# Kernel optimization log

Measured on AMD Instinct MI355X. Metric: run time of the kernel, lower is better.

Reference implementation:

```python
import jax, jax.numpy as jnp
import numpy as np

N = 100000
E = 1600000
F_FEAT, F_COND, F_HID, F_LAT = 128, 32, 128, 64


def setup_inputs() -> dict:
    key = jax.random.key(0)
    ks = jax.random.split(key, 16)
    feature = jax.random.normal(ks[0], (N, F_FEAT), dtype=jnp.float32)
    condition = jax.random.normal(ks[1], (N, F_COND), dtype=jnp.float32)
    edge_index = jax.random.randint(ks[2], (2, E), 0, N, dtype=jnp.int64)

    def glorot(k, fan_in, fan_out):
        s = jnp.sqrt(6.0 / (fan_in + fan_out)).astype(jnp.float32)
        return jax.random.uniform(k, (fan_in, fan_out), jnp.float32, -s, s)

    enc_in = F_FEAT + F_COND   # 160
    dec_in = F_LAT + F_COND    # 96
    return {
        "feature": feature,
        "condition": condition,
        "edge_index": edge_index,
        "W_e1": glorot(ks[3], enc_in, F_HID), "b_e1": jnp.zeros((F_HID,), jnp.float32),
        "W_e2": glorot(ks[4], F_HID, F_HID), "b_e2": jnp.zeros((F_HID,), jnp.float32),
        "W_e3": glorot(ks[5], F_HID, F_LAT), "b_e3": jnp.zeros((F_LAT,), jnp.float32),
        "W_d1": glorot(ks[6], dec_in, F_HID), "b_d1": jnp.zeros((F_HID,), jnp.float32),
        "W_d2": glorot(ks[7], F_HID, F_HID), "b_d2": jnp.zeros((F_HID,), jnp.float32),
        "W_d3": glorot(ks[8], F_HID, F_FEAT), "b_d3": jnp.zeros((F_FEAT,), jnp.float32),
    }


def _gcn_conv(x, W, b, src, dst, dinv):
    # GCNConv with add_self_loops=True, symmetric normalization:
    # out = D^{-1/2} (A + I) D^{-1/2} X W + b
    h = x @ W                                        # [N, out]
    coef = (dinv[src] * dinv[dst])[:, None]          # [E, 1]
    msg = h[src] * coef                              # [E, out]
    agg = jax.ops.segment_sum(msg, dst, num_segments=x.shape[0])
    agg = agg + h * (dinv * dinv)[:, None]           # self-loop term
    return agg + b


def reference(feature, condition, edge_index,
              W_e1, b_e1, W_e2, b_e2, W_e3, b_e3,
              W_d1, b_d1, W_d2, b_d2, W_d3, b_d3):
    src, dst = edge_index[0], edge_index[1]
    n = feature.shape[0]
    # degree with self loops (edge weights = 1)
    deg = jax.ops.segment_sum(jnp.ones((src.shape[0],), jnp.float32), dst,
                              num_segments=n) + 1.0
    dinv = jax.lax.rsqrt(deg)

    # encoder
    x = jnp.concatenate([feature, condition], axis=1)
    h = jnp.tanh(_gcn_conv(x, W_e1, b_e1, src, dst, dinv))
    h = jnp.tanh(_gcn_conv(h, W_e2, b_e2, src, dst, dinv))
    z = _gcn_conv(h, W_e3, b_e3, src, dst, dinv)

    # decoder
    x = jnp.concatenate([z, condition], axis=1)
    h = jnp.tanh(_gcn_conv(x, W_d1, b_d1, src, dst, dinv))
    h = jnp.tanh(_gcn_conv(h, W_d2, b_d2, src, dst, dinv))
    out = _gcn_conv(h, W_d3, b_d3, src, dst, dinv)
    return out
```

## Files before the change

kernel.cpp:

```cpp
#include <hip/hip_runtime.h>
#include <hip/hip_fp16.h>
#include <math.h>

#define NN 100000
#define NE 1600000
#define NB ((NN + 255) >> 8)
#define CHUNK 8192
#define CAP 8192

typedef __attribute__((ext_vector_type(4))) float floatx4;
typedef __attribute__((ext_vector_type(8))) short shortx8;


__global__ __launch_bounds__(256)
void coarse_hist(const int* __restrict__ ei, int* __restrict__ bucket_cnt, int E) {
    __shared__ int h[512];
    int t = threadIdx.x;
    for (int i = t; i < 512; i += 256) h[i] = 0;
    __syncthreads();
    int base = blockIdx.x * CHUNK;
    int lim = min(base + CHUNK, E);
    for (int e = base + t; e < lim; e += 256) {
        int d = ei[E + e];
        atomicAdd(&h[d >> 8], 1);
    }
    __syncthreads();
    for (int i = t; i < 512; i += 256)
        if (h[i]) atomicAdd(&bucket_cnt[i], h[i]);
}

__global__ void scan_buckets(const int* __restrict__ bucket_cnt,
                             int* __restrict__ bucket_base,
                             int* __restrict__ bucket_fill) {
    __shared__ int sh[512];
    int t = threadIdx.x;
    int v = (t < NB) ? bucket_cnt[t] : 0;
    sh[t] = v;
    __syncthreads();
    for (int off = 1; off < 512; off <<= 1) {
        int u = (t >= off) ? sh[t - off] : 0;
        __syncthreads();
        sh[t] += u;
        __syncthreads();
    }
    int ex = (t == 0) ? 0 : sh[t - 1];
    if (t <= NB) bucket_base[t] = ex;
    if (t < NB) bucket_fill[t] = ex;
}

__global__ __launch_bounds__(256)
void coarse_scatter(const int* __restrict__ ei, int* __restrict__ bucket_fill,
                    unsigned long long* __restrict__ pairs, int E) {
    __shared__ int h[512];
    __shared__ int base[512];
    int t = threadIdx.x;
    for (int i = t; i < 512; i += 256) h[i] = 0;
    __syncthreads();
    int cbase = blockIdx.x * CHUNK;
    int lim = min(cbase + CHUNK, E);
    for (int e = cbase + t; e < lim; e += 256) {
        int d = ei[E + e];
        atomicAdd(&h[d >> 8], 1);
    }
    __syncthreads();
    for (int i = t; i < 512; i += 256)
        base[i] = h[i] ? atomicAdd(&bucket_fill[i], h[i]) : 0;
    __syncthreads();
    for (int i = t; i < 512; i += 256) h[i] = 0;
    __syncthreads();
    for (int e = cbase + t; e < lim; e += 256) {
        int s = ei[e];
        int d = ei[E + e];
        int b = d >> 8;
        int r = atomicAdd(&h[b], 1);
        pairs[base[b] + r] =
            ((unsigned long long)(unsigned)d << 32) | (unsigned)s;
    }
}

__global__ __launch_bounds__(256)
void fine_csr(const unsigned long long* __restrict__ pairs,
              const int* __restrict__ bucket_base,
              int* __restrict__ rowptr, int* __restrict__ colid,
              float* __restrict__ dinv, int n) {
    __shared__ int hist[256];
    __shared__ int offs[256];
    __shared__ int rank[256];
    __shared__ int lbuf[CAP];
    int b = blockIdx.x, t = threadIdx.x;
    int beg = bucket_base[b], end = bucket_base[b + 1];
    int cnt = end - beg;
    hist[t] = 0; rank[t] = 0;
    __syncthreads();
    for (int i = t; i < cnt; i += 256) {
        int d = (int)(pairs[beg + i] >> 32);
        atomicAdd(&hist[d & 255], 1);
    }
    __syncthreads();
    int v = hist[t];
    offs[t] = v;
    __syncthreads();
    for (int off = 1; off < 256; off <<= 1) {
        int u = (t >= off) ? offs[t - off] : 0;
        __syncthreads();
        offs[t] += u;
        __syncthreads();
    }
    int ex = (t == 0) ? 0 : offs[t - 1];
    int node = (b << 8) + t;
    if (node < n) {
        rowptr[node] = beg + ex;
        dinv[node] = rsqrtf((float)v + 1.0f);
    } else if (node == n) {
        rowptr[n] = beg + ex;
    }
    __syncthreads();
    offs[t] = ex;
    __syncthreads();
    for (int i = t; i < cnt; i += 256) {
        unsigned long long p = pairs[beg + i];
        int d = (int)(p >> 32) & 255;
        int s = (int)(p & 0xffffffffu);
        int r = atomicAdd(&rank[d], 1);
        lbuf[offs[d] + r] = s;
    }
    __syncthreads();
    for (int i = t; i < cnt; i += 256) colid[beg + i] = lbuf[i];
}


__device__ __forceinline__ void wsplit_one(const float* __restrict__ W,
                                           unsigned short* __restrict__ Wsw,
                                           int i, int K, int OUT) {
    int k = i / OUT, o = i % OUT;
    float w = W[i];
    unsigned u = __float_as_uint(w);
    float r = w - __uint_as_float(u & 0xFFFF0000u);
    int NT = OUT >> 4;
    int ktc = k >> 5, q = (k >> 3) & 3, j = k & 7;
    int nt = o >> 4, mm = o & 15;
    int lane = (q << 4) | mm;
    size_t base = ((((size_t)(ktc * NT + nt) * 2) * 64 + lane) << 3) + j;
    Wsw[base] = (unsigned short)(u >> 16);
    Wsw[base + 512] = (unsigned short)(__float_as_uint(r) >> 16);
}

__global__ __launch_bounds__(256)
void wsplit_all(const float* __restrict__ W0, unsigned short* __restrict__ O0,
                const float* __restrict__ W1, unsigned short* __restrict__ O1,
                const float* __restrict__ W2, unsigned short* __restrict__ O2,
                const float* __restrict__ W3, unsigned short* __restrict__ O3,
                const float* __restrict__ W4, unsigned short* __restrict__ O4,
                const float* __restrict__ W5, unsigned short* __restrict__ O5) {
    int i = blockIdx.x * 256 + threadIdx.x;
    if (i < 20480) { wsplit_one(W0, O0, i, 160, 128); return; }
    i -= 20480;
    if (i < 16384) { wsplit_one(W1, O1, i, 128, 128); return; }
    i -= 16384;
    if (i < 8192)  { wsplit_one(W2, O2, i, 128, 64);  return; }
    i -= 8192;
    if (i < 12288) { wsplit_one(W3, O3, i, 96, 128);  return; }
    i -= 12288;
    if (i < 16384) { wsplit_one(W4, O4, i, 128, 128); return; }
    i -= 16384;
    if (i < 16384) { wsplit_one(W5, O5, i, 128, 128); }
}


__device__ __forceinline__ void split8(const float* v, shortx8& hi, shortx8& lo) {
#pragma unroll
    for (int i = 0; i < 8; i++) {
        unsigned u = __float_as_uint(v[i]);
        float r = v[i] - __uint_as_float(u & 0xFFFF0000u);
        hi[i] = (short)(u >> 16);
        lo[i] = (short)(__float_as_uint(r) >> 16);
    }
}

template <int OUT, int K, int K1>
__global__ __launch_bounds__(512, 4)
void gemm_mfma(const float* __restrict__ X1, const float* __restrict__ X2,
               const unsigned short* __restrict__ Wsw,
               const float* __restrict__ dinv,
               __half* __restrict__ Y, int ntiles) {
    constexpr int NT = OUT / 16;
    constexpr int NKTC = K / 32;
    constexpr int K2 = K - K1;
    constexpr int PERC = OUT * 128;
    constexpr int CSZ = (65536 / PERC < NKTC) ? (65536 / PERC) : NKTC;
    __shared__ __align__(16) unsigned short lds[CSZ * PERC / 2];

    const int t = threadIdx.x;
    const int wave = t >> 6, lane = t & 63;
    const int m = lane & 15, q = lane >> 4;
    const int tile0 = blockIdx.x * 16 + wave * 2;
    const int tile1 = tile0 + 1;
    const bool act0 = tile0 < ntiles;
    const bool act1 = tile1 < ntiles;
    const int r0 = act0 ? tile0 * 16 + m : 0;
    const int r1 = act1 ? tile1 * 16 + m : 0;
    const float* ap1a = X1 + (size_t)r0 * K1 + q * 8;
    const float* ap1b = X1 + (size_t)r1 * K1 + q * 8;
    const float* ap2a = (K2 > 0) ? (X2 + (size_t)r0 * K2 + q * 8) : X1;
    const float* ap2b = (K2 > 0) ? (X2 + (size_t)r1 * K2 + q * 8) : X1;

    floatx4 acc0[NT], acc1[NT];
#pragma unroll
    for (int nt = 0; nt < NT; nt++) {
        acc0[nt] = (floatx4){0.f, 0.f, 0.f, 0.f};
        acc1[nt] = (floatx4){0.f, 0.f, 0.f, 0.f};
    }

#pragma unroll
    for (int c0 = 0; c0 < NKTC; c0 += CSZ) {
        const int cl = (NKTC - c0 < CSZ) ? (NKTC - c0) : CSZ;
        if (c0 != 0) __syncthreads();
        {
            const float4* gs = (const float4*)Wsw + (size_t)c0 * (PERC / 16);
            float4* ld = (float4*)lds;
            int tot = cl * (PERC / 16);
            for (int i = t; i < tot; i += 512) ld[i] = gs[i];
        }
        __syncthreads();
#pragma unroll
        for (int ktc = 0; ktc < cl; ktc++) {
            const int kg = (c0 + ktc) * 32;
            const float* pa = (kg < K1) ? (ap1a + kg) : (ap2a + (kg - K1));
            const float* pb = (kg < K1) ? (ap1b + kg) : (ap2b + (kg - K1));
            float av0[8], av1[8];
            *(float4*)&av0[0] = *(const float4*)(pa);
            *(float4*)&av0[4] = *(const float4*)(pa + 4);
            *(float4*)&av1[0] = *(const float4*)(pb);
            *(float4*)&av1[4] = *(const float4*)(pb + 4);
            shortx8 ahi0, alo0, ahi1, alo1;
            split8(av0, ahi0, alo0);
            split8(av1, ahi1, alo1);
#pragma unroll
            for (int nt = 0; nt < NT; nt++) {
                const unsigned short* fb =
                    lds + ((((ktc * NT + nt) * 2) * 64 + lane) << 3);
                shortx8 bhi = *(const shortx8*)fb;
                shortx8 blo = *(const shortx8*)(fb + 512);
                acc0[nt] = __builtin_amdgcn_mfma_f32_16x16x32_bf16(ahi0, bhi, acc0[nt], 0, 0, 0);
                acc1[nt] = __builtin_amdgcn_mfma_f32_16x16x32_bf16(ahi1, bhi, acc1[nt], 0, 0, 0);
                acc0[nt] = __builtin_amdgcn_mfma_f32_16x16x32_bf16(ahi0, blo, acc0[nt], 0, 0, 0);
                acc1[nt] = __builtin_amdgcn_mfma_f32_16x16x32_bf16(ahi1, blo, acc1[nt], 0, 0, 0);
                acc0[nt] = __builtin_amdgcn_mfma_f32_16x16x32_bf16(alo0, bhi, acc0[nt], 0, 0, 0);
                acc1[nt] = __builtin_amdgcn_mfma_f32_16x16x32_bf16(alo1, bhi, acc1[nt], 0, 0, 0);
            }
        }
    }

    if (act0) {
        float di[4];
#pragma unroll
        for (int r = 0; r < 4; r++) di[r] = dinv[tile0 * 16 + q * 4 + r];
#pragma unroll
        for (int nt = 0; nt < NT; nt++) {
#pragma unroll
            for (int r = 0; r < 4; r++) {
                int orow = tile0 * 16 + q * 4 + r;
                Y[(size_t)orow * OUT + nt * 16 + m] =
                    __float2half_rn(acc0[nt][r] * di[r]);
            }
        }
    }
    if (act1) {
        float di[4];
#pragma unroll
        for (int r = 0; r < 4; r++) di[r] = dinv[tile1 * 16 + q * 4 + r];
#pragma unroll
        for (int nt = 0; nt < NT; nt++) {
#pragma unroll
            for (int r = 0; r < 4; r++) {
                int orow = tile1 * 16 + q * 4 + r;
                Y[(size_t)orow * OUT + nt * 16 + m] =
                    __float2half_rn(acc1[nt][r] * di[r]);
            }
        }
    }
}


template <int OUT, bool TANH>
__global__ __launch_bounds__(256)
void prop_row(const __half2* __restrict__ hs, const float* __restrict__ dinv,
              const int* __restrict__ rowptr, const int* __restrict__ colid,
              const float* __restrict__ bias, float* __restrict__ out,
              int ldo, int n) {
    constexpr int LPR = OUT / 4;
    constexpr int G = 64 / LPR;
    constexpr int RS2 = OUT / 4;

    int wave = threadIdx.x >> 6, lane = threadIdx.x & 63;
    int node = blockIdx.x * 4 + wave;
    if (node >= n) return;
    int g = lane / LPR, fq = lane % LPR;
    int beg = rowptr[node], end = rowptr[node + 1];
    const float2* __restrict__ b2 = (const float2*)hs;

    float ax = 0.f, ay = 0.f, az = 0.f, aw = 0.f;
    int e = beg;
    for (; e + 8 * G <= end; e += 8 * G) {
        int s[8];
#pragma unroll
        for (int j = 0; j < 8; j++) s[j] = colid[e + j * G + g];
        float2 v[8];
#pragma unroll
        for (int j = 0; j < 8; j++) v[j] = b2[(size_t)s[j] * RS2 + fq];
#pragma unroll
        for (int j = 0; j < 8; j++) {
            float2 f0 = __half22float2(*(const __half2*)&v[j].x);
            float2 f1 = __half22float2(*(const __half2*)&v[j].y);
            ax += f0.x; ay += f0.y; az += f1.x; aw += f1.y;
        }
    }
    if (e + 4 * G <= end) {
        int s[4];
#pragma unroll
        for (int j = 0; j < 4; j++) s[j] = colid[e + j * G + g];
        float2 v[4];
#pragma unroll
        for (int j = 0; j < 4; j++) v[j] = b2[(size_t)s[j] * RS2 + fq];
#pragma unroll
        for (int j = 0; j < 4; j++) {
            float2 f0 = __half22float2(*(const __half2*)&v[j].x);
            float2 f1 = __half22float2(*(const __half2*)&v[j].y);
            ax += f0.x; ay += f0.y; az += f1.x; aw += f1.y;
        }
        e += 4 * G;
    }
    for (; e + G <= end; e += G) {
        int s = colid[e + g];
        float2 v = b2[(size_t)s * RS2 + fq];
        float2 f0 = __half22float2(*(const __half2*)&v.x);
        float2 f1 = __half22float2(*(const __half2*)&v.y);
        ax += f0.x; ay += f0.y; az += f1.x; aw += f1.y;
    }
    if (e + g < end) {
        int s = colid[e + g];
        float2 v = b2[(size_t)s * RS2 + fq];
        float2 f0 = __half22float2(*(const __half2*)&v.x);
        float2 f1 = __half22float2(*(const __half2*)&v.y);
        ax += f0.x; ay += f0.y; az += f1.x; aw += f1.y;
    }

    if constexpr (G >= 2) {
        ax += __shfl_xor(ax, LPR); ay += __shfl_xor(ay, LPR);
        az += __shfl_xor(az, LPR); aw += __shfl_xor(aw, LPR);
    }
    if constexpr (G == 4) {
        ax += __shfl_xor(ax, 2 * LPR); ay += __shfl_xor(ay, 2 * LPR);
        az += __shfl_xor(az, 2 * LPR); aw += __shfl_xor(aw, 2 * LPR);
    }

    if (g == 0) {
        float2 sv = b2[(size_t)node * RS2 + fq];
        float2 f0 = __half22float2(*(const __half2*)&sv.x);
        float2 f1 = __half22float2(*(const __half2*)&sv.y);
        ax += f0.x; ay += f0.y; az += f1.x; aw += f1.y;
        float di = dinv[node];
        float4 bb = *(const float4*)(bias + fq * 4);
        float ox = di * ax + bb.x;
        float oy = di * ay + bb.y;
        float oz = di * az + bb.z;
        float ow = di * aw + bb.w;
        if (TANH) { ox = tanhf(ox); oy = tanhf(oy); oz = tanhf(oz); ow = tanhf(ow); }
        *(float4*)(out + (size_t)node * ldo + fq * 4) = make_float4(ox, oy, oz, ow);
    }
}


extern "C" void kernel_launch(void* const* d_in, const int* in_sizes, int n_in,
                              void* d_out, int out_size, void* d_ws, size_t ws_size,
                              hipStream_t stream) {
    const int n = NN, E = NE;
    const float* feature   = (const float*)d_in[0];
    const float* condition = (const float*)d_in[1];
    const int*   ei        = (const int*)d_in[2];
    const float* W_e1 = (const float*)d_in[3];  const float* b_e1 = (const float*)d_in[4];
    const float* W_e2 = (const float*)d_in[5];  const float* b_e2 = (const float*)d_in[6];
    const float* W_e3 = (const float*)d_in[7];  const float* b_e3 = (const float*)d_in[8];
    const float* W_d1 = (const float*)d_in[9];  const float* b_d1 = (const float*)d_in[10];
    const float* W_d2 = (const float*)d_in[11]; const float* b_d2 = (const float*)d_in[12];
    const float* W_d3 = (const float*)d_in[13]; const float* b_d3 = (const float*)d_in[14];
    float* out = (float*)d_out;

    float*  A    = (float*)d_ws;
    __half* H16  = (__half*)(A + (size_t)n * 160);
    float*  dinv = (float*)(H16 + (size_t)n * 128);
    int* rowptr  = (int*)(dinv + n);
    int* colid   = rowptr + n + 1;
    uintptr_t pp = (uintptr_t)(colid + E);
    pp = (pp + 15) & ~(uintptr_t)15;
    unsigned long long* pairs = (unsigned long long*)pp;
    int* bucket_cnt  = (int*)(pairs + E);
    int* bucket_base = bucket_cnt + 512;
    int* bucket_fill = bucket_base + 512;
    uintptr_t wp = (uintptr_t)(bucket_fill + 512);
    wp = (wp + 15) & ~(uintptr_t)15;
    unsigned short* wt = (unsigned short*)wp;
    unsigned short* e1w = wt;              unsigned short* e2w = e1w + 160 * 128 * 2;
    unsigned short* e3w = e2w + 128*128*2; unsigned short* d1w = e3w + 128 * 64 * 2;
    unsigned short* d2w = d1w + 96*128*2;  unsigned short* d3w = d2w + 128 * 128 * 2;

    hipMemsetAsync(bucket_cnt, 0, 512 * sizeof(int), stream);

    int nbc = (E + CHUNK - 1) / CHUNK;
    coarse_hist<<<nbc, 256, 0, stream>>>(ei, bucket_cnt, E);
    scan_buckets<<<1, 512, 0, stream>>>(bucket_cnt, bucket_base, bucket_fill);
    coarse_scatter<<<nbc, 256, 0, stream>>>(ei, bucket_fill, pairs, E);
    fine_csr<<<NB, 256, 0, stream>>>(pairs, bucket_base, rowptr, colid, dinv, n);

    wsplit_all<<<(90112 + 255) / 256, 256, 0, stream>>>(
        W_e1, e1w, W_e2, e2w, W_e3, e3w, W_d1, d1w, W_d2, d2w, W_d3, d3w);

    const int ntiles = n / 16;
    const int gb = (ntiles + 15) / 16;
    const int pb = (n + 3) / 4;

    gemm_mfma<128, 160, 128><<<gb, 512, 0, stream>>>(feature, condition, e1w, dinv, H16, ntiles);
    prop_row<128, true><<<pb, 256, 0, stream>>>((const __half2*)H16, dinv, rowptr, colid, b_e1, A, 128, n);
    gemm_mfma<128, 128, 128><<<gb, 512, 0, stream>>>(A, nullptr, e2w, dinv, H16, ntiles);
    prop_row<128, true><<<pb, 256, 0, stream>>>((const __half2*)H16, dinv, rowptr, colid, b_e2, A, 128, n);
    gemm_mfma<64, 128, 128><<<gb, 512, 0, stream>>>(A, nullptr, e3w, dinv, H16, ntiles);
    prop_row<64, false><<<pb, 256, 0, stream>>>((const __half2*)H16, dinv, rowptr, colid, b_e3, A, 64, n);

    gemm_mfma<128, 96, 64><<<gb, 512, 0, stream>>>(A, condition, d1w, dinv, H16, ntiles);
    prop_row<128, true><<<pb, 256, 0, stream>>>((const __half2*)H16, dinv, rowptr, colid, b_d1, A, 128, n);
    gemm_mfma<128, 128, 128><<<gb, 512, 0, stream>>>(A, nullptr, d2w, dinv, H16, ntiles);
    prop_row<128, true><<<pb, 256, 0, stream>>>((const __half2*)H16, dinv, rowptr, colid, b_d2, A, 128, n);
    gemm_mfma<128, 128, 128><<<gb, 512, 0, stream>>>(A, nullptr, d3w, dinv, H16, ntiles);
    prop_row<128, false><<<pb, 256, 0, stream>>>((const __half2*)H16, dinv, rowptr, colid, b_d3, out, 128, n);
}
```

Measured before the change: 691.2 us.

## Fuse graph propagation with the following layer's MFMA GEMM per 16-node tile

Adds a fused_pg kernel that gathers neighbor rows for 16 nodes into LDS as split bf16 hi/lo, applies bias and tanh, and immediately runs the next layer's weight GEMM with MFMA. It writes fp16 prescaled outputs, ping-ponging between two half buffers. This removes the fp32 intermediate activation round-trip through global memory and halves the kernel launches between layers. In exchange each block handles only 16 nodes and reads weights from global memory per wave, which may limit occupancy and reuse.

```diff
diff --git a/kernel.cpp b/kernel.cpp
--- a/kernel.cpp
+++ b/kernel.cpp
@@ -256,27 +256,189 @@
 #pragma unroll
         for (int r = 0; r < 4; r++) di[r] = dinv[tile0 * 16 + q * 4 + r];
 #pragma unroll
-        for (int nt = 0; nt < NT; nt++) {
+        for (int nt = 0; nt < NT; nt++)
 #pragma unroll
             for (int r = 0; r < 4; r++) {
                 int orow = tile0 * 16 + q * 4 + r;
                 Y[(size_t)orow * OUT + nt * 16 + m] =
                     __float2half_rn(acc0[nt][r] * di[r]);
             }
-        }
     }
     if (act1) {
         float di[4];
 #pragma unroll
         for (int r = 0; r < 4; r++) di[r] = dinv[tile1 * 16 + q * 4 + r];
 #pragma unroll
-        for (int nt = 0; nt < NT; nt++) {
+        for (int nt = 0; nt < NT; nt++)
 #pragma unroll
             for (int r = 0; r < 4; r++) {
                 int orow = tile1 * 16 + q * 4 + r;
                 Y[(size_t)orow * OUT + nt * 16 + m] =
                     __float2half_rn(acc1[nt][r] * di[r]);
             }
+    }
+}
+
+
+template <int INW, int OUT, bool CC, bool TANH>
+__global__ __launch_bounds__(256, 4)
+void fused_pg(const __half2* __restrict__ hin, const float* __restrict__ dinv,
+              const int* __restrict__ rowptr, const int* __restrict__ colid,
+              const float* __restrict__ biasIn, const float* __restrict__ cond,
+              const unsigned short* __restrict__ Wsw,
+              __half* __restrict__ hout, int n) {
+    constexpr int KG = CC ? INW + 32 : INW;
+    constexpr int NT = OUT / 16;
+    constexpr int NTW = NT / 4;
+    constexpr int NKTC = KG / 32;
+    constexpr int LPR = INW / 4;
+    constexpr int G = 64 / LPR;
+    constexpr int RS2 = INW / 4;
+
+    __shared__ __align__(16) unsigned char xlds[8192];
+
+    const int t = threadIdx.x;
+    const int wave = t >> 6, lane = t & 63;
+    const int blk = blockIdx.x;
+    const int g = lane / LPR, fq = lane % LPR;
+    const float2* __restrict__ b2 = (const float2*)hin;
+
+    for (int nd = 0; nd < 4; nd++) {
+        int node = blk * 16 + wave * 4 + nd;
+        int beg = rowptr[node], end = rowptr[node + 1];
+        float ax = 0.f, ay = 0.f, az = 0.f, aw = 0.f;
+        int e = beg;
+        for (; e + 8 * G <= end; e += 8 * G) {
+            int s[8];
+#pragma unroll
+            for (int j = 0; j < 8; j++) s[j] = colid[e + j * G + g];
+            float2 v[8];
+#pragma unroll
+            for (int j = 0; j < 8; j++) v[j] = b2[(size_t)s[j] * RS2 + fq];
+#pragma unroll
+            for (int j = 0; j < 8; j++) {
+                float2 f0 = __half22float2(*(const __half2*)&v[j].x);
+                float2 f1 = __half22float2(*(const __half2*)&v[j].y);
+                ax += f0.x; ay += f0.y; az += f1.x; aw += f1.y;
+            }
+        }
+        if (e + 4 * G <= end) {
+            int s[4];
+#pragma unroll
+            for (int j = 0; j < 4; j++) s[j] = colid[e + j * G + g];
+            float2 v[4];
+#pragma unroll
+            for (int j = 0; j < 4; j++) v[j] = b2[(size_t)s[j] * RS2 + fq];
+#pragma unroll
+            for (int j = 0; j < 4; j++) {
+                float2 f0 = __half22float2(*(const __half2*)&v[j].x);
+                float2 f1 = __half22float2(*(const __half2*)&v[j].y);
+                ax += f0.x; ay += f0.y; az += f1.x; aw += f1.y;
+            }
+            e += 4 * G;
+        }
+        for (; e + G <= end; e += G) {
+            int s = colid[e + g];
+            float2 v = b2[(size_t)s * RS2 + fq];
+            float2 f0 = __half22float2(*(const __half2*)&v.x);
+            float2 f1 = __half22float2(*(const __half2*)&v.y);
+            ax += f0.x; ay += f0.y; az += f1.x; aw += f1.y;
+        }
+        if (e + g < end) {
+            int s = colid[e + g];
+            float2 v = b2[(size_t)s * RS2 + fq];
+            float2 f0 = __half22float2(*(const __half2*)&v.x);
+            float2 f1 = __half22float2(*(const __half2*)&v.y);
+            ax += f0.x; ay += f0.y; az += f1.x; aw += f1.y;
+        }
+        if constexpr (G >= 2) {
+            ax += __shfl_xor(ax, LPR); ay += __shfl_xor(ay, LPR);
+            az += __shfl_xor(az, LPR); aw += __shfl_xor(aw, LPR);
+        }
+        if constexpr (G == 4) {
+            ax += __shfl_xor(ax, 2 * LPR); ay += __shfl_xor(ay, 2 * LPR);
+            az += __shfl_xor(az, 2 * LPR); aw += __shfl_xor(aw, 2 * LPR);
+        }
+        const int r = wave * 4 + nd;
+        if (g == 0) {
+            float2 sv = b2[(size_t)node * RS2 + fq];
+            float2 f0 = __half22float2(*(const __half2*)&sv.x);
+            float2 f1 = __half22float2(*(const __half2*)&sv.y);
+            ax += f0.x; ay += f0.y; az += f1.x; aw += f1.y;
+            float di = dinv[node];
+            float4 bb = *(const float4*)(biasIn + fq * 4);
+            float o0 = di * ax + bb.x;
+            float o1 = di * ay + bb.y;
+            float o2 = di * az + bb.z;
+            float o3 = di * aw + bb.w;
+            if (TANH) { o0 = tanhf(o0); o1 = tanhf(o1); o2 = tanhf(o2); o3 = tanhf(o3); }
+            float o[4] = {o0, o1, o2, o3};
+            unsigned short hi[4], lo[4];
+#pragma unroll
+            for (int i = 0; i < 4; i++) {
+                unsigned u = __float_as_uint(o[i]);
+                float rr = o[i] - __uint_as_float(u & 0xFFFF0000u);
+                hi[i] = (unsigned short)(u >> 16);
+                lo[i] = (unsigned short)(__float_as_uint(rr) >> 16);
+            }
+            int off = (r * 256 + fq * 8) ^ ((r & 7) << 4);
+            *(uint2*)(xlds + off) = *(const uint2*)hi;
+            *(uint2*)(xlds + 4096 + off) = *(const uint2*)lo;
+        }
+        if constexpr (CC) {
+            if (g == 1 && fq < 8) {
+                float4 cv = ((const float4*)cond)[(size_t)node * 8 + fq];
+                float c[4] = {cv.x, cv.y, cv.z, cv.w};
+                unsigned short hi[4], lo[4];
+#pragma unroll
+                for (int i = 0; i < 4; i++) {
+                    unsigned u = __float_as_uint(c[i]);
+                    float rr = c[i] - __uint_as_float(u & 0xFFFF0000u);
+                    hi[i] = (unsigned short)(u >> 16);
+                    lo[i] = (unsigned short)(__float_as_uint(rr) >> 16);
+                }
+                int off = (r * 256 + 128 + fq * 8) ^ ((r & 7) << 4);
+                *(uint2*)(xlds + off) = *(const uint2*)hi;
+                *(uint2*)(xlds + 4096 + off) = *(const uint2*)lo;
+            }
+        }
+    }
+    __syncthreads();
+
+    const int m = lane & 15, q = lane >> 4;
+    floatx4 acc[NTW];
+#pragma unroll
+    for (int j = 0; j < NTW; j++) acc[j] = (floatx4){0.f, 0.f, 0.f, 0.f};
+
+#pragma unroll
+    for (int kc = 0; kc < NKTC; kc++) {
+        int rdoff = (m * 256 + kc * 64 + q * 16) ^ ((m & 7) << 4);
+        shortx8 ahi = *(const shortx8*)(xlds + rdoff);
+        shortx8 alo = *(const shortx8*)(xlds + 4096 + rdoff);
+#pragma unroll
+        for (int j = 0; j < NTW; j++) {
+            int nt = wave * NTW + j;
+            const unsigned short* wp =
+                Wsw + ((((size_t)(kc * NT + nt) * 2) * 64 + lane) << 3);
+            shortx8 whi = *(const shortx8*)wp;
+            shortx8 wlo = *(const shortx8*)(wp + 512);
+            acc[j] = __builtin_amdgcn_mfma_f32_16x16x32_bf16(ahi, whi, acc[j], 0, 0, 0);
+            acc[j] = __builtin_amdgcn_mfma_f32_16x16x32_bf16(ahi, wlo, acc[j], 0, 0, 0);
+            acc[j] = __builtin_amdgcn_mfma_f32_16x16x32_bf16(alo, whi, acc[j], 0, 0, 0);
+        }
+    }
+
+    float di[4];
+#pragma unroll
+    for (int r = 0; r < 4; r++) di[r] = dinv[blk * 16 + q * 4 + r];
+#pragma unroll
+    for (int j = 0; j < NTW; j++) {
+        int nt = wave * NTW + j;
+#pragma unroll
+        for (int r = 0; r < 4; r++) {
+            int orow = blk * 16 + q * 4 + r;
+            hout[(size_t)orow * OUT + nt * 16 + m] =
+                __float2half_rn(acc[j][r] * di[r]);
         }
     }
 }
@@ -387,8 +549,9 @@
     float* out = (float*)d_out;
 
     float*  A    = (float*)d_ws;
-    __half* H16  = (__half*)(A + (size_t)n * 160);
-    float*  dinv = (float*)(H16 + (size_t)n * 128);
+    __half* H16a = (__half*)(A + (size_t)n * 160);
+    __half* H16b = (__half*)A;
+    float*  dinv = (float*)(H16a + (size_t)n * 128);
     int* rowptr  = (int*)(dinv + n);
     int* colid   = rowptr + n + 1;
     uintptr_t pp = (uintptr_t)(colid + E);
@@ -417,19 +580,20 @@
 
     const int ntiles = n / 16;
     const int gb = (ntiles + 15) / 16;
+    const int fb = ntiles;
     const int pb = (n + 3) / 4;
 
-    gemm_mfma<128, 160, 128><<<gb, 512, 0, stream>>>(feature, condition, e1w, dinv, H16, ntiles);
-    prop_row<128, true><<<pb, 256, 0, stream>>>((const __half2*)H16, dinv, rowptr, colid, b_e1, A, 128, n);
-    gemm_mfma<128, 128, 128><<<gb, 512, 0, stream>>>(A, nullptr, e2w, dinv, H16, ntiles);
-    prop_row<128, true><<<pb, 256, 0, stream>>>((const __half2*)H16, dinv, rowptr, colid, b_e2, A, 128, n);
-    gemm_mfma<64, 128, 128><<<gb, 512, 0, stream>>>(A, nullptr, e3w, dinv, H16, ntiles);
-    prop_row<64, false><<<pb, 256, 0, stream>>>((const __half2*)H16, dinv, rowptr, colid, b_e3, A, 64, n);
-
-    gemm_mfma<128, 96, 64><<<gb, 512, 0, stream>>>(A, condition, d1w, dinv, H16, ntiles);
-    prop_row<128, true><<<pb, 256, 0, stream>>>((const __half2*)H16, dinv, rowptr, colid, b_d1, A, 128, n);
-    gemm_mfma<128, 128, 128><<<gb, 512, 0, stream>>>(A, nullptr, d2w, dinv, H16, ntiles);
-    prop_row<128, true><<<pb, 256, 0, stream>>>((const __half2*)H16, dinv, rowptr, colid, b_d2, A, 128, n);
-    gemm_mfma<128, 128, 128><<<gb, 512, 0, stream>>>(A, nullptr, d3w, dinv, H16, ntiles);
-    prop_row<128, false><<<pb, 256, 0, stream>>>((const __half2*)H16, dinv, rowptr, colid, b_d3, out, 128, n);
-}
+    gemm_mfma<128, 160, 128><<<gb, 512, 0, stream>>>(feature, condition, e1w, dinv, H16a, ntiles);
+    fused_pg<128, 128, false, true><<<fb, 256, 0, stream>>>(
+        (const __half2*)H16a, dinv, rowptr, colid, b_e1, nullptr, e2w, H16b, n);
+    fused_pg<128, 64, false, true><<<fb, 256, 0, stream>>>(
+        (const __half2*)H16b, dinv, rowptr, colid, b_e2, nullptr, e3w, H16a, n);
+    fused_pg<64, 128, true, false><<<fb, 256, 0, stream>>>(
+        (const __half2*)H16a, dinv, rowptr, colid, b_e3, condition, d1w, H16b, n);
+    fused_pg<128, 128, false, true><<<fb, 256, 0, stream>>>(
+        (const __half2*)H16b, dinv, rowptr, colid, b_d1, nullptr, d2w, H16a, n);
+    fused_pg<128, 128, false, true><<<fb, 256, 0, stream>>>(
+        (const __half2*)H16a, dinv, rowptr, colid, b_d2, nullptr, d3w, H16b, n);
+    prop_row<128, false><<<pb, 256, 0, stream>>>(
+        (const __half2*)H16b, dinv, rowptr, colid, b_d3, out, 128, n);
+}
```

Measured after the change: 669.4 us. 3.2% less time.
